# Optimization experiments

Hardware: AMD Instinct MI355X
Metric: run time of the kernel (lower is better)

The kernel has to match this reference:

```python
import jax, jax.numpy as jnp
import numpy as np

H, DM, DK, DV, DFF = 8, 512, 64, 64, 2048
B, S = 8, 1024
EPS = 1e-5


def layernorm_global(x):
    # torch nn.LayerNorm(x.size()[1:], elementwise_affine=False): normalize over ALL dims except batch
    mu = jnp.mean(x, axis=(1, 2), keepdims=True)
    var = jnp.var(x, axis=(1, 2), keepdims=True)
    return (x - mu) / jnp.sqrt(var + EPS)


def mha(q_in, k_in, v_in, wq, bq, wk, bk, wv, bv, wo, bo, causal):
    # wq/wk: [h, dk, dmodel], wv: [h, dv, dmodel] (torch Linear weight layout [out,in])
    q = jnp.einsum('bsd,hkd->bhsk', q_in, wq) + bq[None, :, None, :]
    k = jnp.einsum('bsd,hkd->bhsk', k_in, wk) + bk[None, :, None, :]
    v = jnp.einsum('bsd,hvd->bhsv', v_in, wv) + bv[None, :, None, :]
    scores = jnp.einsum('bhqk,bhsk->bhqs', q, k) / np.sqrt(DK).astype(np.float32)
    if causal:
        Sq = q_in.shape[1]
        mask = jnp.triu(jnp.full((Sq, Sq), -jnp.inf, dtype=scores.dtype), k=1)
        scores = scores + mask[None, None, :, :]
    w = jax.nn.softmax(scores, axis=-1)
    attn = jnp.einsum('bhqs,bhsv->bhqv', w, v)  # [b,h,q,dv]
    concat = attn.transpose(0, 2, 1, 3).reshape(q_in.shape[0], q_in.shape[1], H * DV)
    return concat @ wo.T + bo


def setup_inputs() -> dict:
    key = jax.random.key(0)
    ks = jax.random.split(key, 24)
    f = lambda k, shape: (jax.random.normal(k, shape, dtype=jnp.float32) * 0.02)
    inp = {
        'x_enc': jax.random.normal(ks[0], (B, S, DM), dtype=jnp.float32),
        'x_dec': jax.random.normal(ks[1], (B, S, DM), dtype=jnp.float32),
        # masked self-attention params
        'mq_w': f(ks[2], (H, DK, DM)), 'mq_b': f(ks[3], (H, DK)),
        'mk_w': f(ks[4], (H, DK, DM)), 'mk_b': f(ks[5], (H, DK)),
        'mv_w': f(ks[6], (H, DV, DM)), 'mv_b': f(ks[7], (H, DV)),
        'mo_w': f(ks[8], (DM, H * DV)), 'mo_b': f(ks[9], (DM,)),
        # cross-attention params
        'cq_w': f(ks[10], (H, DK, DM)), 'cq_b': f(ks[11], (H, DK)),
        'ck_w': f(ks[12], (H, DK, DM)), 'ck_b': f(ks[13], (H, DK)),
        'cv_w': f(ks[14], (H, DV, DM)), 'cv_b': f(ks[15], (H, DV)),
        'co_w': f(ks[16], (DM, H * DV)), 'co_b': f(ks[17], (DM,)),
        # feedforward params
        'f1_w': f(ks[18], (DFF, DM)), 'f1_b': f(ks[19], (DFF,)),
        'f2_w': f(ks[20], (DM, DFF)), 'f2_b': f(ks[21], (DM,)),
    }
    return inp


def reference(x_enc, x_dec,
              mq_w, mq_b, mk_w, mk_b, mv_w, mv_b, mo_w, mo_b,
              cq_w, cq_b, ck_w, ck_b, cv_w, cv_b, co_w, co_b,
              f1_w, f1_b, f2_w, f2_b):
    # masked self-attention block (dropout = identity at eval)
    x_dec_n = layernorm_global(x_dec)
    sa = mha(x_dec_n, x_dec_n, x_dec_n, mq_w, mq_b, mk_w, mk_b, mv_w, mv_b, mo_w, mo_b, causal=True)
    current = x_dec + sa
    # cross-attention block
    cur_n = layernorm_global(current)
    enc_n = layernorm_global(x_enc)
    ca = mha(cur_n, enc_n, enc_n, cq_w, cq_b, ck_w, ck_b, cv_w, cv_b, co_w, co_b, causal=False)
    result = current + ca
    # feedforward block
    res_n = layernorm_global(result)
    ff = jax.nn.relu(res_n @ f1_w.T + f1_b) @ f2_w.T + f2_b
    return result + ff
```

## Files before the change

### kernel.cpp

```cpp
#include <hip/hip_runtime.h>
#include <cmath>
#include <cstddef>
#include <cstdint>

#define BN   8
#define SN   1024
#define DMN  512
#define HN   8
#define DKN  64
#define DFFN 2048

typedef short           bf16x8   __attribute__((ext_vector_type(8)));
typedef float           f32x4    __attribute__((ext_vector_type(4)));
typedef float           f32x16   __attribute__((ext_vector_type(16)));
typedef unsigned short  ushortx4 __attribute__((ext_vector_type(4)));
typedef unsigned short  ushortx8 __attribute__((ext_vector_type(8)));
typedef unsigned int    uintx4   __attribute__((ext_vector_type(4)));
typedef unsigned short  u16;
typedef unsigned int    u32;

#define ATT_SC 0.18033688011112042f

__device__ __forceinline__ float bf2f(u16 u) {
  return __uint_as_float(((unsigned int)u) << 16);
}
__device__ __forceinline__ u16 f2bf(float f) {
  unsigned int u = __float_as_uint(f);
  u += 0x7FFFu + ((u >> 16) & 1u);
  return (u16)(u >> 16);
}
__device__ __forceinline__ u32 cvtpk_bf16(float lo, float hi) {
  u32 r;
  asm("v_cvt_pk_bf16_f32 %0, %1, %2" : "=v"(r) : "v"(lo), "v"(hi));
  return r;
}
__device__ __forceinline__ void gload_lds16(const u16* gsrc, u16* ldst) {
  __builtin_amdgcn_global_load_lds(
      (const __attribute__((address_space(1))) unsigned int*)gsrc,
      (__attribute__((address_space(3))) unsigned int*)ldst,
      16, 0, 0);
}
__device__ __forceinline__ int xcd_swz(int lid, int nwg) {
  const int cpx = nwg >> 3;
  return (lid & 7) * cpx + (lid >> 3);
}

__global__ __launch_bounds__(256) void cvt_weights(
    const float* p0, const float* p1, const float* p2, const float* p3,
    const float* p4, const float* p5, const float* p6, const float* p7,
    const float* p8, const float* p9, u16* __restrict__ dst) {
  const int gi = blockIdx.x * 256 + threadIdx.x;
  const int idx = gi * 4;
  const float* src; int off;
  if (idx < 2097152) {
    const int t = idx >> 18; off = idx & 262143;
    switch (t) {
      case 0: src = p0; break; case 1: src = p1; break;
      case 2: src = p2; break; case 3: src = p3; break;
      case 4: src = p4; break; case 5: src = p5; break;
      case 6: src = p6; break; default: src = p7; break;
    }
  } else if (idx < 3145728) { src = p8; off = idx - 2097152; }
  else                      { src = p9; off = idx - 3145728; }
  float4 v = *(const float4*)(src + off);
  ushortx4 o;
  o[0] = f2bf(v.x); o[1] = f2bf(v.y); o[2] = f2bf(v.z); o[3] = f2bf(v.w);
  *(ushortx4*)(dst + idx) = o;
}

__global__ __launch_bounds__(256) void pack_bias(const float* a, const float* b,
                                                 const float* c, const float* d,
                                                 const float* e, float* __restrict__ dst) {
  const int t = threadIdx.x;
#pragma unroll
  for (int i = t; i < 512; i += 256) {
    dst[i]        = a[i];
    dst[512 + i]  = b[i];
    dst[1024 + i] = c[i];
    dst[1536 + i] = d[i];
    dst[2048 + i] = e[i];
  }
}

template<bool INBF>
__device__ __forceinline__ void ln_sum_body(const void* Xv_, float2* part, int g, int b, int t) {
  float s = 0.f, s2 = 0.f;
  if (INBF) {
    const ushortx8* Xv = (const ushortx8*)((const u16*)Xv_ + (size_t)b * (SN * DMN) + (size_t)g * 8192);
#pragma unroll
    for (int it = 0; it < 4; ++it) {
      ushortx8 x = Xv[t + it * 256];
#pragma unroll
      for (int e = 0; e < 8; ++e) { float f = bf2f(x[e]); s += f; s2 += f * f; }
    }
  } else {
    const float4* Xv = (const float4*)((const float*)Xv_ + (size_t)b * (SN * DMN) + (size_t)g * 8192);
#pragma unroll
    for (int it = 0; it < 8; ++it) {
      float4 x = Xv[t + it * 256];
      s  += x.x + x.y + x.z + x.w;
      s2 += x.x*x.x + x.y*x.y + x.z*x.z + x.w*x.w;
    }
  }
  __shared__ float rs[256], rq[256];
  rs[t] = s; rq[t] = s2;
  __syncthreads();
  for (int off = 128; off > 0; off >>= 1) {
    if (t < off) { rs[t] += rs[t + off]; rq[t] += rq[t + off]; }
    __syncthreads();
  }
  if (t == 0) part[b * 64 + g] = make_float2(rs[0], rq[0]);
}

template<bool INBF>
__device__ __forceinline__ void ln_norm_body(const void* Xv_, const float2* part,
                                             u16* Y, int g, int b, int t) {
  __shared__ float ss[64], sq[64];
  if (t < 64) { float2 p = part[b * 64 + t]; ss[t] = p.x; sq[t] = p.y; }
  __syncthreads();
  float s = 0.f, q = 0.f;
#pragma unroll
  for (int j = 0; j < 64; ++j) { s += ss[j]; q += sq[j]; }
  const float inv_n = 1.f / (float)(SN * DMN);
  const float mu = s * inv_n;
  const float var = q * inv_n - mu * mu;
  const float rstd = rsqrtf(var + 1e-5f);
  const size_t base = (size_t)b * (SN * DMN) + (size_t)g * 8192;
  if (INBF) {
    const ushortx8* Xv = (const ushortx8*)((const u16*)Xv_ + base);
#pragma unroll
    for (int it = 0; it < 4; ++it) {
      ushortx8 x = Xv[t + it * 256];
      ushortx8 o;
#pragma unroll
      for (int e = 0; e < 8; ++e) o[e] = f2bf((bf2f(x[e]) - mu) * rstd);
      *(ushortx8*)(Y + base + (size_t)(t + it * 256) * 8) = o;
    }
  } else {
    const float4* Xv = (const float4*)((const float*)Xv_ + base);
#pragma unroll
    for (int it = 0; it < 8; ++it) {
      float4 x = Xv[t + it * 256];
      ushortx4 o;
      o[0] = f2bf((x.x - mu) * rstd); o[1] = f2bf((x.y - mu) * rstd);
      o[2] = f2bf((x.z - mu) * rstd); o[3] = f2bf((x.w - mu) * rstd);
      *(ushortx4*)(Y + base + (size_t)(t + it * 256) * 4) = o;
    }
  }
}

template<bool INBF>
__global__ __launch_bounds__(256) void ln_sum(const void* __restrict__ Xv_,
                                              float2* __restrict__ part) {
  ln_sum_body<INBF>(Xv_, part, blockIdx.x, blockIdx.y, threadIdx.x);
}
template<bool INBF>
__global__ __launch_bounds__(256) void ln_norm(const void* __restrict__ Xv_,
                                               const float2* __restrict__ part,
                                               u16* __restrict__ Y) {
  ln_norm_body<INBF>(Xv_, part, Y, blockIdx.x, blockIdx.y, threadIdx.x);
}
__global__ __launch_bounds__(256) void ln_sum2(const void* __restrict__ X0,
                                               const void* __restrict__ X1,
                                               float2* __restrict__ part) {
  if (blockIdx.z == 0) ln_sum_body<true>(X0, part, blockIdx.x, blockIdx.y, threadIdx.x);
  else                 ln_sum_body<false>(X1, part + 512, blockIdx.x, blockIdx.y, threadIdx.x);
}
__global__ __launch_bounds__(256) void ln_norm2(const void* __restrict__ X0,
                                                const void* __restrict__ X1,
                                                const float2* __restrict__ part,
                                                u16* __restrict__ Y0,
                                                u16* __restrict__ Y1) {
  if (blockIdx.z == 0) ln_norm_body<true>(X0, part, Y0, blockIdx.x, blockIdx.y, threadIdx.x);
  else                 ln_norm_body<false>(X1, part + 512, Y1, blockIdx.x, blockIdx.y, threadIdx.x);
}

template<bool RELU, bool RES, bool RESBF, int OMODE, int BM, bool QSC>
__global__ __launch_bounds__(256) void gemm_mfma(const u16* __restrict__ A,
                                                 const u16* __restrict__ W,
                                                 const float* __restrict__ bias,
                                                 const void* __restrict__ resv,
                                                 void* __restrict__ Cv,
                                                 void* __restrict__ Cv2,
                                                 void* __restrict__ Cv3,
                                                 int M, int N, int K) {
  constexpr int MI = BM / 32;
  __shared__ u16 As[BM * 64];
  __shared__ u16 Bs[128 * 64];
  const int t = threadIdx.x;
  const int lane = t & 63, w = t >> 6;
  const int wm = w >> 1, wn = w & 1;

  const int gx = gridDim.x;
  const int lid = xcd_swz(blockIdx.y * gx + blockIdx.x, gx * gridDim.y);
  const int m0 = (lid / gx) * BM, n0 = (lid % gx) * 128;

  f32x4 acc[MI][4];
#pragma unroll
  for (int i = 0; i < MI; ++i)
#pragma unroll
    for (int j = 0; j < 4; ++j)
      acc[i][j] = (f32x4){0.f, 0.f, 0.f, 0.f};

  const int srow = lane >> 3;
  const int scol = ((lane & 7) ^ (lane >> 3)) * 8;
  const int l15 = lane & 15, l4q = lane >> 4, l7 = lane & 7;

  for (int k0 = 0; k0 < K; k0 += 64) {
#pragma unroll
    for (int c = 0; c < BM / 32; ++c) {
      const int r0 = c * 32 + w * 8;
      gload_lds16(A + (size_t)(m0 + r0 + srow) * K + k0 + scol, &As[r0 * 64]);
    }
#pragma unroll
    for (int c = 0; c < 4; ++c) {
      const int r0 = c * 32 + w * 8;
      gload_lds16(W + (size_t)(n0 + r0 + srow) * K + k0 + scol, &Bs[r0 * 64]);
    }
    __syncthreads();
#pragma unroll
    for (int ks = 0; ks < 2; ++ks) {
      const int kofs = ((ks * 4 + l4q) ^ l7) * 8;
      bf16x8 af[MI], bfr[4];
#pragma unroll
      for (int f = 0; f < MI; ++f)
        af[f]  = *(const bf16x8*)&As[(wm * (BM / 2) + f * 16 + l15) * 64 + kofs];
#pragma unroll
      for (int f = 0; f < 4; ++f)
        bfr[f] = *(const bf16x8*)&Bs[(wn * 64 + f * 16 + l15) * 64 + kofs];
#pragma unroll
      for (int i = 0; i < MI; ++i)
#pragma unroll
        for (int j = 0; j < 4; ++j)
          acc[i][j] = __builtin_amdgcn_mfma_f32_16x16x32_bf16(af[i], bfr[j], acc[i][j], 0, 0, 0);
    }
    __syncthreads();
  }

  const int crow0 = (lane >> 4) * 4;
  const int ccol  = lane & 15;
  float bv[4];
#pragma unroll
  for (int j = 0; j < 4; ++j) bv[j] = bias[n0 + wn * 64 + j * 16 + ccol];

  u16* seg_out = nullptr;
  int  seg_n0 = 0;
  bool seg_vt = false;
  if (OMODE == 3) {
    if (n0 < 512)       { seg_out = (u16*)Cv;  seg_n0 = 0; }
    else if (n0 < 1024) { seg_out = (u16*)Cv2; seg_n0 = 512; }
    else                { seg_out = (u16*)Cv3; seg_n0 = 1024; seg_vt = true; }
  } else if (OMODE == 4) {
    if (n0 < 512)       { seg_out = (u16*)Cv;  seg_n0 = 0; }
    else                { seg_out = (u16*)Cv3; seg_n0 = 512; seg_vt = true; }
  }
  const bool do_scale = QSC && (OMODE != 3 || n0 < 512);

#pragma unroll
  for (int i = 0; i < MI; ++i) {
#pragma unroll
    for (int r = 0; r < 4; ++r) {
      const int m = m0 + wm * (BM / 2) + i * 16 + crow0 + r;
#pragma unroll
      for (int j = 0; j < 4; ++j) {
        const int n = n0 + wn * 64 + j * 16 + ccol;
        float v = acc[i][j][r] + bv[j];
        if (RELU) v = fmaxf(v, 0.f);
        if (RES) {
          if (RESBF) v += bf2f(((const u16*)resv)[(size_t)m * N + n]);
          else       v += ((const float*)resv)[(size_t)m * N + n];
        }
        if (do_scale) v *= ATT_SC;
        if (OMODE == 0) {
          ((float*)Cv)[(size_t)m * N + n] = v;
        } else if (OMODE == 1) {
          ((u16*)Cv)[(size_t)m * N + n] = f2bf(v);
        } else {
          const int nn = n - seg_n0;
          if (!seg_vt) seg_out[(size_t)m * 512 + nn] = f2bf(v);
          else
            seg_out[(((size_t)(m >> 10) * HN + (nn >> 6)) * 64 + (nn & 63)) * SN + (m & 1023)] = f2bf(v);
        }
      }
    }
  }
}

#define QBLK 128
#define KVB  64

template<int CAUSAL, int NSPLIT>
__global__ __launch_bounds__(256) void attn_mfma(const u16* __restrict__ Q,
                                                 const u16* __restrict__ K,
                                                 const u16* __restrict__ VT,
                                                 u16* __restrict__ Out,
                                                 float* __restrict__ Lbuf) {
  const int lid = xcd_swz(blockIdx.y * 8 + blockIdx.x, 512);
  const int qb = lid & 7;
  const int bh = lid >> 3;
  const int sp = (NSPLIT > 1) ? blockIdx.z : 0;
  const int b = bh >> 3, h = bh & 7;
  const int t = threadIdx.x;
  const int lane = t & 63, w = t >> 6;
  const int l31 = lane & 31, hi = lane >> 5;

  __shared__ __align__(16) u16 Ks[64 * 64];
  __shared__ __align__(16) u16 Vts[8 * 512];

  const int qw0 = qb * QBLK + w * 32;
  const int qglob = qw0 + l31;

  bf16x8 bq[4];
#pragma unroll
  for (int dk = 0; dk < 4; ++dk)
    bq[dk] = *(const bf16x8*)(Q + (size_t)(b * SN + qglob) * 512
                                + h * 64 + dk * 16 + hi * 8);

  f32x16 acc0 = {}, acc1 = {};
  float l_run = 0.f;

  const int ntile = CAUSAL ? (2 * qb + 2) : (SN / KVB);
  const int n4 = (ntile + NSPLIT - 1) / NSPLIT;
  const int kt0 = sp * n4;
  const int ktend = (kt0 + n4 < ntile) ? (kt0 + n4) : ntile;

  const int srow = t >> 2;
  const int ss0  = 2 * (t & 3);
  const u16* kg0 = K + (size_t)(b * SN + srow) * 512 + h * 64 + ((ss0 ^ (srow & 7)) * 8)
                     + (size_t)kt0 * KVB * 512;
  const u16* kg1 = K + (size_t)(b * SN + srow) * 512 + h * 64 + (((ss0 + 1) ^ (srow & 7)) * 8)
                     + (size_t)kt0 * KVB * 512;
  u16* kd0 = &Ks[t * 16];
  u16* kd1 = &Ks[t * 16 + 8];
  const int vd = t & 63, vp = t >> 6;
  const u16* vg = VT + ((size_t)bh * 64 + vd) * SN + vp * 16 + kt0 * KVB;
  u16* vdst0 = &Vts[(2 * vp) * 512 + vd * 8];
  u16* vdst1 = &Vts[(2 * vp + 1) * 512 + vd * 8];

  ushortx8 kr0, kr1, vr0, vr1;
  kr0 = *(const ushortx8*)kg0;
  kr1 = *(const ushortx8*)kg1;
  vr0 = *(const ushortx8*)vg;
  vr1 = *(const ushortx8*)(vg + 8);
  kg0 += (size_t)KVB * 512; kg1 += (size_t)KVB * 512; vg += KVB;

  for (int kt = kt0; kt < ktend; ++kt) {
    const int k0 = kt * KVB;
    __syncthreads();
    *(ushortx8*)kd0 = kr0;
    *(ushortx8*)kd1 = kr1;
    {
      ushortx8 sl, sh;
#pragma unroll
      for (int e = 0; e < 4; ++e) {
        sl[e] = vr0[e];     sl[e + 4] = vr1[e];
        sh[e] = vr0[e + 4]; sh[e + 4] = vr1[e + 4];
      }
      *(ushortx8*)vdst0 = sl;
      *(ushortx8*)vdst1 = sh;
    }
    if (kt + 1 < ktend) {
      kr0 = *(const ushortx8*)kg0;
      kr1 = *(const ushortx8*)kg1;
      vr0 = *(const ushortx8*)vg;
      vr1 = *(const ushortx8*)(vg + 8);
      kg0 += (size_t)KVB * 512; kg1 += (size_t)KVB * 512; vg += KVB;
    }
    __syncthreads();

    if (CAUSAL && k0 > qw0 + 31) continue;

    f32x16 s0 = {}, s1 = {};
    __builtin_amdgcn_s_setprio(1);
#pragma unroll
    for (int dk = 0; dk < 4; ++dk) {
      const int boff = dk * 32 + hi * 16;
      const int sw = boff ^ ((l31 & 7) << 4);
      bf16x8 a0 = *(const bf16x8*)&Ks[l31 * 64 + (sw >> 1)];
      bf16x8 a1 = *(const bf16x8*)&Ks[(32 + l31) * 64 + (sw >> 1)];
      s0 = __builtin_amdgcn_mfma_f32_32x32x16_bf16(a0, bq[dk], s0, 0, 0, 0);
      s1 = __builtin_amdgcn_mfma_f32_32x32x16_bf16(a1, bq[dk], s1, 0, 0, 0);
    }
    __builtin_amdgcn_s_setprio(0);

    if (CAUSAL && (k0 + KVB - 1 > qw0)) {
#pragma unroll
      for (int i = 0; i < 16; ++i) {
        const int krow = (i & 3) + 8 * (i >> 2) + 4 * hi;
        if (k0 + krow > qglob)      s0[i] = -INFINITY;
        if (k0 + 32 + krow > qglob) s1[i] = -INFINITY;
      }
    }
    float ps = 0.f;
#pragma unroll
    for (int i = 0; i < 16; ++i) {
      s0[i] = exp2f(s0[i]); ps += s0[i];
      s1[i] = exp2f(s1[i]); ps += s1[i];
    }
    l_run += ps;

    __builtin_amdgcn_s_setprio(1);
#pragma unroll
    for (int m = 0; m < 4; ++m) {
      uintx4 pw;
      if (m == 0) {
        pw[0] = cvtpk_bf16(s0[0], s0[1]);  pw[1] = cvtpk_bf16(s0[2], s0[3]);
        pw[2] = cvtpk_bf16(s0[4], s0[5]);  pw[3] = cvtpk_bf16(s0[6], s0[7]);
      } else if (m == 1) {
        pw[0] = cvtpk_bf16(s0[8], s0[9]);  pw[1] = cvtpk_bf16(s0[10], s0[11]);
        pw[2] = cvtpk_bf16(s0[12], s0[13]); pw[3] = cvtpk_bf16(s0[14], s0[15]);
      } else if (m == 2) {
        pw[0] = cvtpk_bf16(s1[0], s1[1]);  pw[1] = cvtpk_bf16(s1[2], s1[3]);
        pw[2] = cvtpk_bf16(s1[4], s1[5]);  pw[3] = cvtpk_bf16(s1[6], s1[7]);
      } else {
        pw[0] = cvtpk_bf16(s1[8], s1[9]);  pw[1] = cvtpk_bf16(s1[10], s1[11]);
        pw[2] = cvtpk_bf16(s1[12], s1[13]); pw[3] = cvtpk_bf16(s1[14], s1[15]);
      }
      const bf16x8 pb = *(const bf16x8*)&pw;
      const bf16x8 av0 = *(const bf16x8*)&Vts[(m * 2 + hi) * 512 + l31 * 8];
      const bf16x8 av1 = *(const bf16x8*)&Vts[(m * 2 + hi) * 512 + (32 + l31) * 8];
      acc0 = __builtin_amdgcn_mfma_f32_32x32x16_bf16(av0, pb, acc0, 0, 0, 0);
      acc1 = __builtin_amdgcn_mfma_f32_32x32x16_bf16(av1, pb, acc1, 0, 0, 0);
    }
    __builtin_amdgcn_s_setprio(0);
  }

  l_run += __shfl_xor(l_run, 32);
  if (NSPLIT == 1) {
    const float inv = 1.f / l_run;
    u16* op = Out + (size_t)(b * SN + qglob) * 512 + h * 64;
#pragma unroll
    for (int g = 0; g < 4; ++g) {
      ushortx4 o0, o1;
#pragma unroll
      for (int r = 0; r < 4; ++r) {
        o0[r] = f2bf(acc0[4*g + r] * inv);
        o1[r] = f2bf(acc1[4*g + r] * inv);
      }
      *(ushortx4*)(op + 4*hi + 8*g)      = o0;
      *(ushortx4*)(op + 32 + 4*hi + 8*g) = o1;
    }
  } else {
    u16* op = Out + (((size_t)(sp * 64 + bh)) * 1024 + qglob) * 64;
#pragma unroll
    for (int g = 0; g < 4; ++g) {
      ushortx4 o0, o1;
#pragma unroll
      for (int r = 0; r < 4; ++r) {
        o0[r] = f2bf(acc0[4*g + r]);
        o1[r] = f2bf(acc1[4*g + r]);
      }
      *(ushortx4*)(op + 4*hi + 8*g)      = o0;
      *(ushortx4*)(op + 32 + 4*hi + 8*g) = o1;
    }
    if (hi == 0)
      Lbuf[((size_t)(sp * 64 + bh)) * 1024 + qglob] = l_run;
  }
}

__global__ __launch_bounds__(256) void attn_merge2(const u16* __restrict__ Pacc,
                                                   const float* __restrict__ Lbuf,
                                                   u16* __restrict__ O) {
  const int tid = blockIdx.x * 256 + threadIdx.x;
  const int qh = tid >> 3;
  const int d0 = (tid & 7) * 8;
  const int bh = qh >> 10, q = qh & 1023;
  const int b = bh >> 3, h = bh & 7;

  const float l = Lbuf[(size_t)bh * 1024 + q] + Lbuf[(size_t)(64 + bh) * 1024 + q];
  const float inv = 1.f / l;
  ushortx8 a0 = *(const ushortx8*)(Pacc + ((size_t)bh * 1024 + q) * 64 + d0);
  ushortx8 a1 = *(const ushortx8*)(Pacc + ((size_t)(64 + bh) * 1024 + q) * 64 + d0);
  ushortx8 ov;
#pragma unroll
  for (int e = 0; e < 8; ++e)
    ov[e] = f2bf((bf2f(a0[e]) + bf2f(a1[e])) * inv);
  *(ushortx8*)(O + ((size_t)(b * 1024 + q) * 512) + h * 64 + d0) = ov;
}

extern "C" void kernel_launch(void* const* d_in, const int* in_sizes, int n_in,
                              void* d_out, int out_size, void* d_ws, size_t ws_size,
                              hipStream_t stream) {
  const float* x_enc = (const float*)d_in[0];
  const float* x_dec = (const float*)d_in[1];
  const float* mq_w = (const float*)d_in[2];  const float* mq_b = (const float*)d_in[3];
  const float* mk_w = (const float*)d_in[4];  const float* mk_b = (const float*)d_in[5];
  const float* mv_w = (const float*)d_in[6];  const float* mv_b = (const float*)d_in[7];
  const float* mo_w = (const float*)d_in[8];  const float* mo_b = (const float*)d_in[9];
  const float* cq_w = (const float*)d_in[10]; const float* cq_b = (const float*)d_in[11];
  const float* ck_w = (const float*)d_in[12]; const float* ck_b = (const float*)d_in[13];
  const float* cv_w = (const float*)d_in[14]; const float* cv_b = (const float*)d_in[15];
  const float* co_w = (const float*)d_in[16]; const float* co_b = (const float*)d_in[17];
  const float* f1_w = (const float*)d_in[18]; const float* f1_b = (const float*)d_in[19];
  const float* f2_w = (const float*)d_in[20]; const float* f2_b = (const float*)d_in[21];
  float* out = (float*)d_out;

  char* wsb = (char*)d_ws;
  u16* o5    = (u16*)(wsb + 0);
  u16* o6    = (u16*)(wsb + (16u << 20));
  u16* Qb    = (u16*)(wsb + (32u << 20));
  u16* Kb    = (u16*)(wsb + (40u << 20));
  u16* VTb   = (u16*)(wsb + (48u << 20));
  u16* B0    = (u16*)(wsb + (56u << 20));
  u16* B1    = (u16*)(wsb + (64u << 20));
  u16* FF1   = (u16*)(wsb + (72u << 20));
  u16* WB    = (u16*)(wsb + (104u << 20));
  float2* part = (float2*)(wsb + (112u << 20));
  float* BC  = (float*)(wsb + (113u << 20));

  u16* Pacc   = FF1;
  float* Lbuf = (float*)B1;

  u16* wb_mq = WB + 0 * 262144;
  u16* wb_mo = WB + 3 * 262144;
  u16* wb_cq = WB + 4 * 262144;
  u16* wb_ck = WB + 5 * 262144;
  u16* wb_co = WB + 7 * 262144;
  u16* wb_f1 = WB + 8 * 262144; u16* wb_f2 = WB + 8 * 262144 + 1048576;

  const int M = BN * SN;
  dim3 ln_grid(64, BN);
  dim3 ln_grid2(64, BN, 2);
  dim3 g512s(512 / 128, M / 64);
  dim3 g1024(1024 / 128, M / 128);
  dim3 g1536(1536 / 128, M / 128);
  dim3 g2048(2048 / 128, M / 128);
  dim3 attn_grid_c(SN / QBLK, BN * HN, 2);
  dim3 attn_grid_x(SN / QBLK, BN * HN, 1);

  cvt_weights<<<4096, 256, 0, stream>>>(mq_w, mk_w, mv_w, mo_w, cq_w, ck_w, cv_w, co_w,
                                        f1_w, f2_w, WB);
  pack_bias<<<1, 256, 0, stream>>>(mq_b, mk_b, mv_b, ck_b, cv_b, BC);

  ln_sum<false><<<ln_grid, 256, 0, stream>>>(x_dec, part);
  ln_norm<false><<<ln_grid, 256, 0, stream>>>(x_dec, part, B0);
  gemm_mfma<false, false, false, 3, 128, true><<<g1536, 256, 0, stream>>>(B0, wb_mq, BC, nullptr,
                                                                          Qb, Kb, VTb, M, 1536, 512);
  attn_mfma<1, 2><<<attn_grid_c, 256, 0, stream>>>(Qb, Kb, VTb, Pacc, Lbuf);
  attn_merge2<<<2048, 256, 0, stream>>>(Pacc, Lbuf, B0);
  gemm_mfma<false, true, false, 1, 64, false><<<g512s, 256, 0, stream>>>(B0, wb_mo, mo_b, x_dec,
                                                                         o5, nullptr, nullptr, M, 512, 512);

  ln_sum2<<<ln_grid2, 256, 0, stream>>>(o5, x_enc, part);
  ln_norm2<<<ln_grid2, 256, 0, stream>>>(o5, x_enc, part, B0, B1);
  gemm_mfma<false, false, false, 1, 64, true><<<g512s, 256, 0, stream>>>(B0, wb_cq, cq_b, nullptr,
                                                                         Qb, nullptr, nullptr, M, 512, 512);
  gemm_mfma<false, false, false, 4, 128, false><<<g1024, 256, 0, stream>>>(B1, wb_ck, BC + 1536, nullptr,
                                                                           Kb, nullptr, VTb, M, 1024, 512);
  attn_mfma<0, 1><<<attn_grid_x, 256, 0, stream>>>(Qb, Kb, VTb, B0, nullptr);
  gemm_mfma<false, true, true, 1, 64, false><<<g512s, 256, 0, stream>>>(B0, wb_co, co_b, o5,
                                                                        o6, nullptr, nullptr, M, 512, 512);

  ln_sum<true><<<ln_grid, 256, 0, stream>>>(o6, part);
  ln_norm<true><<<ln_grid, 256, 0, stream>>>(o6, part, B0);
  gemm_mfma<true, false, false, 1, 128, false><<<g2048, 256, 0, stream>>>(B0, wb_f1, f1_b, nullptr,
                                                                          FF1, nullptr, nullptr, M, 2048, 512);
  gemm_mfma<false, true, true, 0, 64, false><<<g512s, 256, 0, stream>>>(FF1, wb_f2, f2_b, o6,
                                                                        out, nullptr, nullptr, M, 512, 2048);
}
```

Before: 253.3 us.

## Double-buffer LDS tiles in BM=64 GEMMs and attention KV loop

Adds an optional double-buffered LDS path to the GEMM kernel. The next K tile is issued into the alternate buffer while MFMAs run on the current one, so each iteration needs one barrier instead of two. It is enabled only for the BM=64 GEMMs (output projections, cross Q, FF2). The attention kernel likewise gets two K/V LDS buffers, writing the next tile while computing the current one and dropping a barrier per tile. The cost is doubled LDS use, which may reduce occupancy.

```diff
diff --git a/kernel.cpp b/kernel.cpp
--- a/kernel.cpp
+++ b/kernel.cpp
@@ -175,7 +175,7 @@
   else                 ln_norm_body<false>(X1, part + 512, Y1, blockIdx.x, blockIdx.y, threadIdx.x);
 }
 
-template<bool RELU, bool RES, bool RESBF, int OMODE, int BM, bool QSC>
+template<bool RELU, bool RES, bool RESBF, int OMODE, int BM, bool QSC, bool DBUF>
 __global__ __launch_bounds__(256) void gemm_mfma(const u16* __restrict__ A,
                                                  const u16* __restrict__ W,
                                                  const float* __restrict__ bias,
@@ -185,8 +185,9 @@
                                                  void* __restrict__ Cv3,
                                                  int M, int N, int K) {
   constexpr int MI = BM / 32;
-  __shared__ u16 As[BM * 64];
-  __shared__ u16 Bs[128 * 64];
+  constexpr int NB = DBUF ? 2 : 1;
+  __shared__ u16 As[NB][BM * 64];
+  __shared__ u16 Bs[NB][128 * 64];
   const int t = threadIdx.x;
   const int lane = t & 63, w = t >> 6;
   const int wm = w >> 1, wn = w & 1;
@@ -206,35 +207,53 @@
   const int scol = ((lane & 7) ^ (lane >> 3)) * 8;
   const int l15 = lane & 15, l4q = lane >> 4, l7 = lane & 7;
 
-  for (int k0 = 0; k0 < K; k0 += 64) {
+  auto STAGE = [&](int buf, int k0) {
 #pragma unroll
     for (int c = 0; c < BM / 32; ++c) {
       const int r0 = c * 32 + w * 8;
-      gload_lds16(A + (size_t)(m0 + r0 + srow) * K + k0 + scol, &As[r0 * 64]);
+      gload_lds16(A + (size_t)(m0 + r0 + srow) * K + k0 + scol, &As[buf][r0 * 64]);
     }
 #pragma unroll
     for (int c = 0; c < 4; ++c) {
       const int r0 = c * 32 + w * 8;
-      gload_lds16(W + (size_t)(n0 + r0 + srow) * K + k0 + scol, &Bs[r0 * 64]);
-    }
-    __syncthreads();
+      gload_lds16(W + (size_t)(n0 + r0 + srow) * K + k0 + scol, &Bs[buf][r0 * 64]);
+    }
+  };
+  auto COMPUTE = [&](int buf) {
 #pragma unroll
     for (int ks = 0; ks < 2; ++ks) {
       const int kofs = ((ks * 4 + l4q) ^ l7) * 8;
       bf16x8 af[MI], bfr[4];
 #pragma unroll
       for (int f = 0; f < MI; ++f)
-        af[f]  = *(const bf16x8*)&As[(wm * (BM / 2) + f * 16 + l15) * 64 + kofs];
+        af[f]  = *(const bf16x8*)&As[buf][(wm * (BM / 2) + f * 16 + l15) * 64 + kofs];
 #pragma unroll
       for (int f = 0; f < 4; ++f)
-        bfr[f] = *(const bf16x8*)&Bs[(wn * 64 + f * 16 + l15) * 64 + kofs];
+        bfr[f] = *(const bf16x8*)&Bs[buf][(wn * 64 + f * 16 + l15) * 64 + kofs];
 #pragma unroll
       for (int i = 0; i < MI; ++i)
 #pragma unroll
         for (int j = 0; j < 4; ++j)
           acc[i][j] = __builtin_amdgcn_mfma_f32_16x16x32_bf16(af[i], bfr[j], acc[i][j], 0, 0, 0);
     }
+  };
+
+  if (DBUF) {
+    const int nt = K >> 6;
+    STAGE(0, 0);
     __syncthreads();
+    for (int ti = 0; ti < nt; ++ti) {
+      if (ti + 1 < nt) STAGE((ti + 1) & 1, (ti + 1) << 6);
+      COMPUTE(ti & 1);
+      if (ti + 1 < nt) __syncthreads();
+    }
+  } else {
+    for (int k0 = 0; k0 < K; k0 += 64) {
+      STAGE(0, k0);
+      __syncthreads();
+      COMPUTE(0);
+      __syncthreads();
+    }
   }
 
   const int crow0 = (lane >> 4) * 4;
@@ -304,8 +323,8 @@
   const int lane = t & 63, w = t >> 6;
   const int l31 = lane & 31, hi = lane >> 5;
 
-  __shared__ __align__(16) u16 Ks[64 * 64];
-  __shared__ __align__(16) u16 Vts[8 * 512];
+  __shared__ __align__(16) u16 Ks[2][64 * 64];
+  __shared__ __align__(16) u16 Vts[2][8 * 512];
 
   const int qw0 = qb * QBLK + w * 32;
   const int qglob = qw0 + l31;
@@ -323,6 +342,7 @@
   const int n4 = (ntile + NSPLIT - 1) / NSPLIT;
   const int kt0 = sp * n4;
   const int ktend = (kt0 + n4 < ntile) ? (kt0 + n4) : ntile;
+  const int ntk = ktend - kt0;
 
   const int srow = t >> 2;
   const int ss0  = 2 * (t & 3);
@@ -330,99 +350,100 @@
                      + (size_t)kt0 * KVB * 512;
   const u16* kg1 = K + (size_t)(b * SN + srow) * 512 + h * 64 + (((ss0 + 1) ^ (srow & 7)) * 8)
                      + (size_t)kt0 * KVB * 512;
-  u16* kd0 = &Ks[t * 16];
-  u16* kd1 = &Ks[t * 16 + 8];
   const int vd = t & 63, vp = t >> 6;
   const u16* vg = VT + ((size_t)bh * 64 + vd) * SN + vp * 16 + kt0 * KVB;
-  u16* vdst0 = &Vts[(2 * vp) * 512 + vd * 8];
-  u16* vdst1 = &Vts[(2 * vp + 1) * 512 + vd * 8];
 
   ushortx8 kr0, kr1, vr0, vr1;
-  kr0 = *(const ushortx8*)kg0;
-  kr1 = *(const ushortx8*)kg1;
-  vr0 = *(const ushortx8*)vg;
-  vr1 = *(const ushortx8*)(vg + 8);
-  kg0 += (size_t)KVB * 512; kg1 += (size_t)KVB * 512; vg += KVB;
-
-  for (int kt = kt0; kt < ktend; ++kt) {
+  auto LOADREGS = [&]() {
+    kr0 = *(const ushortx8*)kg0;
+    kr1 = *(const ushortx8*)kg1;
+    vr0 = *(const ushortx8*)vg;
+    vr1 = *(const ushortx8*)(vg + 8);
+    kg0 += (size_t)KVB * 512; kg1 += (size_t)KVB * 512; vg += KVB;
+  };
+  auto WRITELDS = [&](int buf) {
+    *(ushortx8*)&Ks[buf][t * 16]     = kr0;
+    *(ushortx8*)&Ks[buf][t * 16 + 8] = kr1;
+    ushortx8 sl, sh;
+#pragma unroll
+    for (int e = 0; e < 4; ++e) {
+      sl[e] = vr0[e];     sl[e + 4] = vr1[e];
+      sh[e] = vr0[e + 4]; sh[e + 4] = vr1[e + 4];
+    }
+    *(ushortx8*)&Vts[buf][(2 * vp) * 512 + vd * 8]     = sl;
+    *(ushortx8*)&Vts[buf][(2 * vp + 1) * 512 + vd * 8] = sh;
+  };
+
+  LOADREGS();
+  WRITELDS(0);
+  if (ntk > 1) LOADREGS();
+  __syncthreads();
+
+  for (int ti = 0; ti < ntk; ++ti) {
+    const int kt = kt0 + ti;
     const int k0 = kt * KVB;
-    __syncthreads();
-    *(ushortx8*)kd0 = kr0;
-    *(ushortx8*)kd1 = kr1;
-    {
-      ushortx8 sl, sh;
-#pragma unroll
-      for (int e = 0; e < 4; ++e) {
-        sl[e] = vr0[e];     sl[e + 4] = vr1[e];
-        sh[e] = vr0[e + 4]; sh[e + 4] = vr1[e + 4];
-      }
-      *(ushortx8*)vdst0 = sl;
-      *(ushortx8*)vdst1 = sh;
-    }
-    if (kt + 1 < ktend) {
-      kr0 = *(const ushortx8*)kg0;
-      kr1 = *(const ushortx8*)kg1;
-      vr0 = *(const ushortx8*)vg;
-      vr1 = *(const ushortx8*)(vg + 8);
-      kg0 += (size_t)KVB * 512; kg1 += (size_t)KVB * 512; vg += KVB;
-    }
-    __syncthreads();
-
-    if (CAUSAL && k0 > qw0 + 31) continue;
-
-    f32x16 s0 = {}, s1 = {};
-    __builtin_amdgcn_s_setprio(1);
-#pragma unroll
-    for (int dk = 0; dk < 4; ++dk) {
-      const int boff = dk * 32 + hi * 16;
-      const int sw = boff ^ ((l31 & 7) << 4);
-      bf16x8 a0 = *(const bf16x8*)&Ks[l31 * 64 + (sw >> 1)];
-      bf16x8 a1 = *(const bf16x8*)&Ks[(32 + l31) * 64 + (sw >> 1)];
-      s0 = __builtin_amdgcn_mfma_f32_32x32x16_bf16(a0, bq[dk], s0, 0, 0, 0);
-      s1 = __builtin_amdgcn_mfma_f32_32x32x16_bf16(a1, bq[dk], s1, 0, 0, 0);
-    }
-    __builtin_amdgcn_s_setprio(0);
-
-    if (CAUSAL && (k0 + KVB - 1 > qw0)) {
+    const int cur = ti & 1;
+    if (ti + 1 < ntk) {
+      WRITELDS(cur ^ 1);
+      if (ti + 2 < ntk) LOADREGS();
+    }
+
+    if (!(CAUSAL && k0 > qw0 + 31)) {
+      f32x16 s0 = {}, s1 = {};
+      __builtin_amdgcn_s_setprio(1);
+#pragma unroll
+      for (int dk = 0; dk < 4; ++dk) {
+        const int boff = dk * 32 + hi * 16;
+        const int sw = boff ^ ((l31 & 7) << 4);
+        bf16x8 a0 = *(const bf16x8*)&Ks[cur][l31 * 64 + (sw >> 1)];
+        bf16x8 a1 = *(const bf16x8*)&Ks[cur][(32 + l31) * 64 + (sw >> 1)];
+        s0 = __builtin_amdgcn_mfma_f32_32x32x16_bf16(a0, bq[dk], s0, 0, 0, 0);
+        s1 = __builtin_amdgcn_mfma_f32_32x32x16_bf16(a1, bq[dk], s1, 0, 0, 0);
+      }
+      __builtin_amdgcn_s_setprio(0);
+
+      if (CAUSAL && (k0 + KVB - 1 > qw0)) {
+#pragma unroll
+        for (int i = 0; i < 16; ++i) {
+          const int krow = (i & 3) + 8 * (i >> 2) + 4 * hi;
+          if (k0 + krow > qglob)      s0[i] = -INFINITY;
+          if (k0 + 32 + krow > qglob) s1[i] = -INFINITY;
+        }
+      }
+      float ps = 0.f;
 #pragma unroll
       for (int i = 0; i < 16; ++i) {
-        const int krow = (i & 3) + 8 * (i >> 2) + 4 * hi;
-        if (k0 + krow > qglob)      s0[i] = -INFINITY;
-        if (k0 + 32 + krow > qglob) s1[i] = -INFINITY;
-      }
-    }
-    float ps = 0.f;
-#pragma unroll
-    for (int i = 0; i < 16; ++i) {
-      s0[i] = exp2f(s0[i]); ps += s0[i];
-      s1[i] = exp2f(s1[i]); ps += s1[i];
-    }
-    l_run += ps;
-
-    __builtin_amdgcn_s_setprio(1);
-#pragma unroll
-    for (int m = 0; m < 4; ++m) {
-      uintx4 pw;
-      if (m == 0) {
-        pw[0] = cvtpk_bf16(s0[0], s0[1]);  pw[1] = cvtpk_bf16(s0[2], s0[3]);
-        pw[2] = cvtpk_bf16(s0[4], s0[5]);  pw[3] = cvtpk_bf16(s0[6], s0[7]);
-      } else if (m == 1) {
-        pw[0] = cvtpk_bf16(s0[8], s0[9]);  pw[1] = cvtpk_bf16(s0[10], s0[11]);
-        pw[2] = cvtpk_bf16(s0[12], s0[13]); pw[3] = cvtpk_bf16(s0[14], s0[15]);
-      } else if (m == 2) {
-        pw[0] = cvtpk_bf16(s1[0], s1[1]);  pw[1] = cvtpk_bf16(s1[2], s1[3]);
-        pw[2] = cvtpk_bf16(s1[4], s1[5]);  pw[3] = cvtpk_bf16(s1[6], s1[7]);
-      } else {
-        pw[0] = cvtpk_bf16(s1[8], s1[9]);  pw[1] = cvtpk_bf16(s1[10], s1[11]);
-        pw[2] = cvtpk_bf16(s1[12], s1[13]); pw[3] = cvtpk_bf16(s1[14], s1[15]);
-      }
-      const bf16x8 pb = *(const bf16x8*)&pw;
-      const bf16x8 av0 = *(const bf16x8*)&Vts[(m * 2 + hi) * 512 + l31 * 8];
-      const bf16x8 av1 = *(const bf16x8*)&Vts[(m * 2 + hi) * 512 + (32 + l31) * 8];
-      acc0 = __builtin_amdgcn_mfma_f32_32x32x16_bf16(av0, pb, acc0, 0, 0, 0);
-      acc1 = __builtin_amdgcn_mfma_f32_32x32x16_bf16(av1, pb, acc1, 0, 0, 0);
-    }
-    __builtin_amdgcn_s_setprio(0);
+        s0[i] = exp2f(s0[i]); ps += s0[i];
+        s1[i] = exp2f(s1[i]); ps += s1[i];
+      }
+      l_run += ps;
+
+      __builtin_amdgcn_s_setprio(1);
+#pragma unroll
+      for (int m = 0; m < 4; ++m) {
+        uintx4 pw;
+        if (m == 0) {
+          pw[0] = cvtpk_bf16(s0[0], s0[1]);  pw[1] = cvtpk_bf16(s0[2], s0[3]);
+          pw[2] = cvtpk_bf16(s0[4], s0[5]);  pw[3] = cvtpk_bf16(s0[6], s0[7]);
+        } else if (m == 1) {
+          pw[0] = cvtpk_bf16(s0[8], s0[9]);  pw[1] = cvtpk_bf16(s0[10], s0[11]);
+          pw[2] = cvtpk_bf16(s0[12], s0[13]); pw[3] = cvtpk_bf16(s0[14], s0[15]);
+        } else if (m == 2) {
+          pw[0] = cvtpk_bf16(s1[0], s1[1]);  pw[1] = cvtpk_bf16(s1[2], s1[3]);
+          pw[2] = cvtpk_bf16(s1[4], s1[5]);  pw[3] = cvtpk_bf16(s1[6], s1[7]);
+        } else {
+          pw[0] = cvtpk_bf16(s1[8], s1[9]);  pw[1] = cvtpk_bf16(s1[10], s1[11]);
+          pw[2] = cvtpk_bf16(s1[12], s1[13]); pw[3] = cvtpk_bf16(s1[14], s1[15]);
+        }
+        const bf16x8 pb = *(const bf16x8*)&pw;
+        const bf16x8 av0 = *(const bf16x8*)&Vts[cur][(m * 2 + hi) * 512 + l31 * 8];
+        const bf16x8 av1 = *(const bf16x8*)&Vts[cur][(m * 2 + hi) * 512 + (32 + l31) * 8];
+        acc0 = __builtin_amdgcn_mfma_f32_32x32x16_bf16(av0, pb, acc0, 0, 0, 0);
+        acc1 = __builtin_amdgcn_mfma_f32_32x32x16_bf16(av1, pb, acc1, 0, 0, 0);
+      }
+      __builtin_amdgcn_s_setprio(0);
+    }
+    if (ti + 1 < ntk) __syncthreads();
   }
 
   l_run += __shfl_xor(l_run, 32);
@@ -534,27 +555,27 @@
 
   ln_sum<false><<<ln_grid, 256, 0, stream>>>(x_dec, part);
   ln_norm<false><<<ln_grid, 256, 0, stream>>>(x_dec, part, B0);
-  gemm_mfma<false, false, false, 3, 128, true><<<g1536, 256, 0, stream>>>(B0, wb_mq, BC, nullptr,
-                                                                          Qb, Kb, VTb, M, 1536, 512);
+  gemm_mfma<false, false, false, 3, 128, true, false><<<g1536, 256, 0, stream>>>(
+      B0, wb_mq, BC, nullptr, Qb, Kb, VTb, M, 1536, 512);
   attn_mfma<1, 2><<<attn_grid_c, 256, 0, stream>>>(Qb, Kb, VTb, Pacc, Lbuf);
   attn_merge2<<<2048, 256, 0, stream>>>(Pacc, Lbuf, B0);
-  gemm_mfma<false, true, false, 1, 64, false><<<g512s, 256, 0, stream>>>(B0, wb_mo, mo_b, x_dec,
-                                                                         o5, nullptr, nullptr, M, 512, 512);
+  gemm_mfma<false, true, false, 1, 64, false, true><<<g512s, 256, 0, stream>>>(
+      B0, wb_mo, mo_b, x_dec, o5, nullptr, nullptr, M, 512, 512);
 
   ln_sum2<<<ln_grid2, 256, 0, stream>>>(o5, x_enc, part);
   ln_norm2<<<ln_grid2, 256, 0, stream>>>(o5, x_enc, part, B0, B1);
-  gemm_mfma<false, false, false, 1, 64, true><<<g512s, 256, 0, stream>>>(B0, wb_cq, cq_b, nullptr,
-                                                                         Qb, nullptr, nullptr, M, 512, 512);
-  gemm_mfma<false, false, false, 4, 128, false><<<g1024, 256, 0, stream>>>(B1, wb_ck, BC + 1536, nullptr,
-                                                                           Kb, nullptr, VTb, M, 1024, 512);
+  gemm_mfma<false, false, false, 1, 64, true, true><<<g512s, 256, 0, stream>>>(
+      B0, wb_cq, cq_b, nullptr, Qb, nullptr, nullptr, M, 512, 512);
+  gemm_mfma<false, false, false, 4, 128, false, false><<<g1024, 256, 0, stream>>>(
+      B1, wb_ck, BC + 1536, nullptr, Kb, nullptr, VTb, M, 1024, 512);
   attn_mfma<0, 1><<<attn_grid_x, 256, 0, stream>>>(Qb, Kb, VTb, B0, nullptr);
-  gemm_mfma<false, true, true, 1, 64, false><<<g512s, 256, 0, stream>>>(B0, wb_co, co_b, o5,
-                                                                        o6, nullptr, nullptr, M, 512, 512);
+  gemm_mfma<false, true, true, 1, 64, false, true><<<g512s, 256, 0, stream>>>(
+      B0, wb_co, co_b, o5, o6, nullptr, nullptr, M, 512, 512);
 
   ln_sum<true><<<ln_grid, 256, 0, stream>>>(o6, part);
   ln_norm<true><<<ln_grid, 256, 0, stream>>>(o6, part, B0);
-  gemm_mfma<true, false, false, 1, 128, false><<<g2048, 256, 0, stream>>>(B0, wb_f1, f1_b, nullptr,
-                                                                          FF1, nullptr, nullptr, M, 2048, 512);
-  gemm_mfma<false, true, true, 0, 64, false><<<g512s, 256, 0, stream>>>(FF1, wb_f2, f2_b, o6,
-                                                                        out, nullptr, nullptr, M, 512, 2048);
-}
+  gemm_mfma<true, false, false, 1, 128, false, false><<<g2048, 256, 0, stream>>>(
+      B0, wb_f1, f1_b, nullptr, FF1, nullptr, nullptr, M, 2048, 512);
+  gemm_mfma<false, true, true, 0, 64, false, true><<<g512s, 256, 0, stream>>>(
+      FF1, wb_f2, f2_b, o6, out, nullptr, nullptr, M, 512, 2048);
+}
```

Result: no change. 253.9 us (+0.2%).
